# Performance work log

Hardware: AMD Instinct MI355X
Metric: run time of the kernel (lower is better)

## Reference

```python
import jax, jax.numpy as jnp
import numpy as np

N = 65536          # nodes
D = 64             # nclasses / head dim
H = 1              # num_heads (forward math requires H == 1)
NITER = 4
NITER_ATTN = 4
KHOP = 2           # npow_attn(=1, hard-coded) + 1
R = 1024           # row-chunk size in residual loss
DEG = 8            # out-degree before symmetrization


def setup_inputs():
    rng = np.random.default_rng(0)
    cols0 = rng.integers(0, N, size=N * DEG).astype(np.int32)
    rows0 = np.repeat(np.arange(N, dtype=np.int32), DEG)
    loop = np.arange(N, dtype=np.int32)
    rows = np.concatenate([rows0, cols0, loop])           # symmetrized + self-loops (A + I)
    cols = np.concatenate([cols0, rows0, loop])
    deg = np.bincount(rows, minlength=N).astype(np.float32)
    vals = (1.0 / np.sqrt(deg[rows] * deg[cols])).astype(np.float32)  # D^-1/2 (A+I) D^-1/2
    key = jax.random.key(0)
    ks = jax.random.split(key, 8)
    sc = 1.0 / np.sqrt(D)
    return {
        "local_preds": jax.random.normal(ks[0], (N, D), jnp.float32),
        "idx": jnp.arange(N, dtype=jnp.int32),
        "adj_rows": jnp.asarray(rows),
        "adj_cols": jnp.asarray(cols),
        "adj_vals": jnp.asarray(vals),
        "Wq_w": jax.random.normal(ks[1], (H * D, D), jnp.float32) * sc,
        "Wq_b": jax.random.normal(ks[2], (H * D,), jnp.float32) * sc,
        "Wk_w": jax.random.normal(ks[3], (H * D, D), jnp.float32) * sc,
        "Wk_b": jax.random.normal(ks[4], (H * D,), jnp.float32) * sc,
        "lin1_w": jax.random.normal(ks[5], (1, NITER), jnp.float32) * sc,
        "lin2_w": jax.random.normal(ks[6], (1, NITER_ATTN), jnp.float32) * sc,
    }


def _spmm(rows, cols, vals, x):
    # sparse (A+I)_norm @ x via gather + segment-sum
    return jax.ops.segment_sum(vals[:, None] * x[cols], rows, num_segments=N)


def _fro(x):
    return jnp.sqrt(jnp.sum(x * x))


def _on_attn(qn, kn, vs, n_norm):
    # On_attention_conv with pre-normalized qn/kn, K_hop = KHOP
    new_vs = vs
    for _ in range(KHOP):
        kv = jnp.einsum('lhm,lhd->hmd', kn, new_vs)
        new_vs = jnp.einsum('nhm,hmd->nhd', qn, kv)
    new_vs = new_vs + vs.sum(axis=0)[None]           # + vs_sum broadcast over rows
    normz = jnp.einsum('nhm,hm->nh', qn, kn.sum(axis=0))[..., None] + n_norm
    return new_vs / normz


def _forward(local_preds, adj_rows, adj_cols, adj_vals, Wq_w, Wq_b, Wk_w, Wk_b, lin1_w, lin2_w):
    preds = local_preds
    query = (preds @ Wq_w.T + Wq_b).reshape(N, H, D)
    key_t = (preds @ Wk_w.T + Wk_b).reshape(N, H, D)
    qn = query / _fro(query)   # global-Frobenius normalization (as in torch.norm(qs, p=2))
    kn = key_t / _fro(key_t)
    beta = lin2_w[0]           # [NITER_ATTN]
    alph = lin1_w[0]           # [NITER]

    # main Hop-Stack iteration (H == 1 collapses the head broadcasts)
    M_list = [preds]
    tmp = preds
    for _ in range(1, NITER):
        qk_list = [tmp]
        qk_tmp = tmp
        for _ in range(1, NITER_ATTN):
            qk_tmp = _on_attn(qn, kn, qk_tmp[:, None, :], N).mean(axis=1)
            qk_list.append(qk_tmp)
        mix = jnp.einsum('k,knd->nd', beta, jnp.stack(qk_list))
        tmp = _spmm(adj_rows, adj_cols, adj_vals, mix)
        M_list.append(tmp)
    preds_out = jnp.einsum('k,knd->nd', alph, jnp.stack(M_list))

    # residual loss (torch.no_grad, N > r branch), computed in closed form per row-chunk
    m2 = [query.mean(axis=1)]
    t = query.mean(axis=1)
    for _ in range(2, NITER_ATTN):
        o = _on_attn(qn, kn, t[:, None, :], N).mean(axis=1)
        t = _spmm(adj_rows, adj_cols, adj_vals, o)
        m2.append(t)
    gq = jnp.einsum('k,knd->nd', beta[1:], jnp.stack(m2))[:, None, :]  # GraphA_q [N,H,D]
    c = N // R
    s = jnp.sqrt(jnp.sum(gq.reshape(c, -1) ** 2, axis=1))       # per-chunk Frobenius norm of qs
    row_chunk = jnp.arange(N) // R
    qn2 = gq * (1.0 / s)[row_chunk][:, None, None]
    normz = jnp.einsum('nhm,hm->nh', qn2, kn.sum(axis=0)) + R   # [N,H]
    G = jnp.einsum('lhm,lhp->hmp', kn, kn)                      # key gram [H,D,D]
    # ||attn||_F^2 summed over all chunks, without materializing [R,H,N]
    t1 = jnp.sum(jnp.einsum('nhm,hmp,nhp->nh', qn2, G, qn2) / normz ** 2)
    c0 = beta[0] - 1.0
    dots = jnp.einsum('ehm,ehm->eh', qn2[adj_rows], kn[adj_cols])  # attn at sparse A entries
    t2 = 2.0 * c0 * jnp.sum(adj_vals[:, None] * dots / normz[adj_rows])
    t3 = c0 ** 2 * H * jnp.sum(adj_vals ** 2)
    loss = jnp.sqrt(t1 + t2 + t3)
    return preds_out, jax.lax.stop_gradient(loss)


def reference(local_preds, idx, adj_rows, adj_cols, adj_vals, Wq_w, Wq_b, Wk_w, Wk_b, lin1_w, lin2_w):
    del idx  # unused by the original forward body
    return _forward(local_preds, adj_rows, adj_cols, adj_vals, Wq_w, Wq_b, Wk_w, Wk_b, lin1_w, lin2_w)
```

## Files before the change

kernel.cpp:

```cpp
#include <hip/hip_runtime.h>

#define NN 65536
#define DD 64
#define ND (NN*DD)
#define E0 (NN*8)
#define B1 128
#define EPB (E0/B1)

enum {
  SM_ACC   = 0,
  SM_SCAL  = 4,
  SM_KSUM  = 24,
  SM_CHUNK = 96,
  SM_T2    = 160,
  SM_KQ    = 2208,
  SM_G     = SM_KQ + 4096,
  SM_C0    = SM_G + 4096,
  SM_H     = SM_C0 + 4240,
  SM_Z     = SM_H + 4096,
  SM_ZF    = SM_Z + 4160,
  SM_C     = SM_ZF + 4160,
  SM_CMIX  = SM_C + 4240,
  SM_CFIN  = SM_CMIX + 4240,
  SM_END   = SM_CFIN + 4240
};

#define GP 512
#define RP 512
#define QKP 1024
#define GRAM_STRIDE 12544

__device__ __forceinline__ void f4arr(float4 v, float* a){ a[0]=v.x; a[1]=v.y; a[2]=v.z; a[3]=v.w; }

__device__ __forceinline__ unsigned short f2bf(float f){
  union{float f;unsigned u;}v; v.f=f;
  unsigned r = v.u + 0x7fffu + ((v.u>>16)&1u);
  return (unsigned short)(r>>16);
}
__device__ __forceinline__ float bf2f(unsigned short h){
  union{unsigned u;float f;}v; v.u=((unsigned)h)<<16; return v.f;
}

__global__ __launch_bounds__(256,4) void k_qk(const float* __restrict__ preds,
    const float* __restrict__ Wq, const float* __restrict__ bq,
    const float* __restrict__ Wk, const float* __restrict__ bk,
    float* __restrict__ qout, float* __restrict__ kout, float* __restrict__ slab)
{
  __shared__ float sWq[64*68];
  __shared__ float sWk[64*68];
  __shared__ float sbq[64], sbk[64], sks[64];
  __shared__ float sred[8];
  int t = threadIdx.x;
  for (int i=t;i<4096;i+=256){ int d=i>>6, m=i&63; sWq[m*68+d]=Wq[i]; sWk[m*68+d]=Wk[i]; }
  if (t<64){ sbq[t]=bq[t]; sbk[t]=bk[t]; sks[t]=0.f; }
  __syncthreads();
  int td=t&15, g=t>>4, d0=td*4;
  int base = blockIdx.x*64;
  float aq[16], ak[16];
  #pragma unroll
  for (int i=0;i<4;i++)
    #pragma unroll
    for (int j=0;j<4;j++){ aq[i*4+j]=sbq[d0+j]; ak[i*4+j]=sbk[d0+j]; }
  const float4* pr0=(const float4*)(preds+(size_t)(base+g   )*DD);
  const float4* pr1=(const float4*)(preds+(size_t)(base+g+16)*DD);
  const float4* pr2=(const float4*)(preds+(size_t)(base+g+32)*DD);
  const float4* pr3=(const float4*)(preds+(size_t)(base+g+48)*DD);
  float4 pc0=pr0[0], pc1=pr1[0], pc2=pr2[0], pc3=pr3[0];
  for (int ms=0; ms<16; ms++){
    float4 pn0=pc0,pn1=pc1,pn2=pc2,pn3=pc3;
    if (ms<15){ pn0=pr0[ms+1]; pn1=pr1[ms+1]; pn2=pr2[ms+1]; pn3=pr3[ms+1]; }
    int m=ms*4;
    float wq[4][4], wk[4][4];
    #pragma unroll
    for (int k=0;k<4;k++){ f4arr(*(const float4*)&sWq[(m+k)*68+d0], wq[k]); f4arr(*(const float4*)&sWk[(m+k)*68+d0], wk[k]); }
    float p[4];
    f4arr(pc0,p);
    #pragma unroll
    for (int k=0;k<4;k++)
      #pragma unroll
      for (int j=0;j<4;j++){ aq[0*4+j]+=p[k]*wq[k][j]; ak[0*4+j]+=p[k]*wk[k][j]; }
    f4arr(pc1,p);
    #pragma unroll
    for (int k=0;k<4;k++)
      #pragma unroll
      for (int j=0;j<4;j++){ aq[1*4+j]+=p[k]*wq[k][j]; ak[1*4+j]+=p[k]*wk[k][j]; }
    f4arr(pc2,p);
    #pragma unroll
    for (int k=0;k<4;k++)
      #pragma unroll
      for (int j=0;j<4;j++){ aq[2*4+j]+=p[k]*wq[k][j]; ak[2*4+j]+=p[k]*wk[k][j]; }
    f4arr(pc3,p);
    #pragma unroll
    for (int k=0;k<4;k++)
      #pragma unroll
      for (int j=0;j<4;j++){ aq[3*4+j]+=p[k]*wq[k][j]; ak[3*4+j]+=p[k]*wk[k][j]; }
    pc0=pn0; pc1=pn1; pc2=pn2; pc3=pn3;
  }
  float ssq=0.f, ssk=0.f;
  #pragma unroll
  for (int i=0;i<4;i++){
    int r=base+g+16*i;
    float4 Q=make_float4(aq[i*4+0],aq[i*4+1],aq[i*4+2],aq[i*4+3]);
    float4 K=make_float4(ak[i*4+0],ak[i*4+1],ak[i*4+2],ak[i*4+3]);
    ((float4*)(qout+(size_t)r*DD))[td]=Q;
    ((float4*)(kout+(size_t)r*DD))[td]=K;
    ssq += Q.x*Q.x+Q.y*Q.y+Q.z*Q.z+Q.w*Q.w;
    ssk += K.x*K.x+K.y*K.y+K.z*K.z+K.w*K.w;
  }
  #pragma unroll
  for (int j=0;j<4;j++){
    float cs = ak[0*4+j]+ak[1*4+j]+ak[2*4+j]+ak[3*4+j];
    atomicAdd(&sks[d0+j], cs);
  }
  #pragma unroll
  for (int off=32;off;off>>=1){ ssq+=__shfl_down(ssq,off,64); ssk+=__shfl_down(ssk,off,64); }
  if ((t&63)==0){ sred[t>>6]=ssq; sred[4+(t>>6)]=ssk; }
  __syncthreads();
  float* my = slab + (size_t)blockIdx.x*66;
  if (t<64) my[t]=sks[t];
  if (t==0){ my[64]=sred[0]+sred[1]+sred[2]+sred[3]; my[65]=sred[4]+sred[5]+sred[6]+sred[7]; }
}

__global__ __launch_bounds__(256) void k_psumW(const float* __restrict__ slab, int stride, int n, int P,
                                               float* __restrict__ out)
{
  int col=blockIdx.x*4+(threadIdx.x>>6);
  int lane=threadIdx.x&63;
  if (col>=n) return;
  float a0=0.f,a1=0.f;
  int p=lane;
  for (; p+64<P; p+=128){ a0+=slab[(size_t)p*stride+col]; a1+=slab[(size_t)(p+64)*stride+col]; }
  for (; p<P; p+=64) a0+=slab[(size_t)p*stride+col];
  float a=a0+a1;
  #pragma unroll
  for (int off=32;off;off>>=1) a+=__shfl_down(a,off,64);
  if (lane==0) out[col]=a;
}

__global__ void k_scalars(float* __restrict__ ksum, float* __restrict__ sc, const float* __restrict__ lin2){
  __shared__ float s_ki;
  int t=threadIdx.x;
  if (t==0){
    float fq=sqrtf(ksum[64]), fk=sqrtf(ksum[65]);
    float qi=1.f/fq, ki=1.f/fk;
    sc[0]=qi; sc[1]=ki; sc[2]=qi*ki; sc[3]=lin2[1]*qi; sc[4]=1.f;
    sc[5]=ki;    sc[6]=1.f; sc[7]=qi;
    sc[8]=qi*ki; sc[9]=qi;  sc[10]=qi;
    s_ki=ki;
  }
  __syncthreads();
  if (t<64) ksum[t]*=s_ki;
}

__global__ __launch_bounds__(256) void k_gramc0p(const float* __restrict__ qn, const float* __restrict__ kn,
    const float* __restrict__ ksum, const float* __restrict__ sc,
    float* __restrict__ invn, float* __restrict__ slab)
{
  __shared__ float sk[16][64], sq[16][64], sw[16], sks[64];
  int t=threadIdx.x, tp=t&15, tm=t>>4;
  if (t<64) sks[t]=ksum[t];
  float qi_=sc[0];
  float akq[16], ag[16], ac0[16];
  #pragma unroll
  for (int i=0;i<16;i++){akq[i]=0.f;ag[i]=0.f;ac0[i]=0.f;}
  float rb[4]={0,0,0,0}, cb[4]={0,0,0,0}; float s22=0.f;
  for (int tile=blockIdx.x; tile<NN/16; tile+=gridDim.x){
    int base=tile*16;
    ((float4*)sk)[t]=((const float4*)(kn+(size_t)base*DD))[t];
    ((float4*)sq)[t]=((const float4*)(qn+(size_t)base*DD))[t];
    __syncthreads();
    {
      float p = sq[tm][tp]*sks[tp] + sq[tm][tp+16]*sks[tp+16]
              + sq[tm][tp+32]*sks[tp+32] + sq[tm][tp+48]*sks[tp+48];
      p += __shfl_xor(p,1,64); p += __shfl_xor(p,2,64);
      p += __shfl_xor(p,4,64); p += __shfl_xor(p,8,64);
      float w = 1.f/(p*qi_ + (float)NN);
      if (tp==0){ sw[tm]=w; invn[base+tm]=w; }
    }
    __syncthreads();
    #pragma unroll
    for (int r=0;r<16;r++){
      float w=sw[r];
      float km[4],qp[4],kp[4];
      f4arr(((const float4*)&sk[r][0])[tm], km);
      f4arr(((const float4*)&sq[r][0])[tp], qp);
      f4arr(((const float4*)&sk[r][0])[tp], kp);
      float wq[4]={w*qp[0],w*qp[1],w*qp[2],w*qp[3]};
      #pragma unroll
      for (int i=0;i<4;i++)
        #pragma unroll
        for (int j=0;j<4;j++){
          akq[i*4+j]+=km[i]*qp[j];
          ag [i*4+j]+=km[i]*kp[j];
          ac0[i*4+j]+=km[i]*wq[j];
        }
      if (tp==0){
        #pragma unroll
        for (int i=0;i<4;i++) rb[i]+=km[i]*w;
      }
      if (tm==0){
        #pragma unroll
        for (int j=0;j<4;j++) cb[j]+=wq[j];
      }
      if (t==0) s22+=w;
    }
    __syncthreads();
  }
  float* my = slab + (size_t)blockIdx.x*GRAM_STRIDE;
  #pragma unroll
  for (int i=0;i<4;i++)
    #pragma unroll
    for (int j=0;j<4;j++){
      my[       (tm*4+i)*DD+tp*4+j] = akq[i*4+j];
      my[4096 + (tm*4+i)*DD+tp*4+j] = ag [i*4+j];
      my[8192 + (tm*4+i)*65+tp*4+j] = ac0[i*4+j];
    }
  if (tp==0){
    #pragma unroll
    for (int i=0;i<4;i++) my[8192 + (tm*4+i)*65+64] = rb[i];
  }
  if (tm==0){
    #pragma unroll
    for (int j=0;j<4;j++) my[8192 + 64*65+tp*4+j] = cb[j];
  }
  if (t==0) my[8192 + 64*65+64] = s22;
}

__global__ void k_applyscale(float* __restrict__ KQ, float* __restrict__ G, float* __restrict__ C0,
                             const float* __restrict__ sc){
  int i=blockIdx.x*256+threadIdx.x;
  float qi=sc[0], ki=sc[1], qk=sc[2];
  if (i<4096){ KQ[i]*=qk; G[i]*=ki*ki; }
  if (i<4225){
    int a=i/65, b=i-65*a;
    float s = (a<64)? (b<64? qk : ki) : (b<64? qi : 1.f);
    C0[i]*=s;
  }
}

__global__ __launch_bounds__(256) void k_Hp(const float* __restrict__ q2, const float* __restrict__ wv,
                                            float* __restrict__ slab)
{
  __shared__ float sq[16][64], sw[16];
  int t=threadIdx.x, tp=t&15, tm=t>>4;
  float acc[16];
  #pragma unroll
  for (int i=0;i<16;i++) acc[i]=0.f;
  for (int tile=blockIdx.x; tile<NN/16; tile+=gridDim.x){
    int base=tile*16;
    ((float4*)sq)[t]=((const float4*)(q2+(size_t)base*DD))[t];
    if (t<16) sw[t]=wv[base+t];
    __syncthreads();
    #pragma unroll
    for (int r=0;r<16;r++){
      float w=sw[r]; w=w*w;
      float qm[4],qp[4];
      f4arr(((const float4*)&sq[r][0])[tm], qm);
      f4arr(((const float4*)&sq[r][0])[tp], qp);
      float wq[4]={w*qp[0],w*qp[1],w*qp[2],w*qp[3]};
      #pragma unroll
      for (int i=0;i<4;i++)
        #pragma unroll
        for (int j=0;j<4;j++) acc[i*4+j]+=qm[i]*wq[j];
    }
    __syncthreads();
  }
  float* my = slab + (size_t)blockIdx.x*4096;
  #pragma unroll
  for (int i=0;i<4;i++)
    #pragma unroll
    for (int j=0;j<4;j++) my[(tm*4+i)*DD+tp*4+j] = acc[i*4+j];
}

__global__ __launch_bounds__(256) void k_redp(const float* __restrict__ kn, const float* __restrict__ v,
                                              float* __restrict__ slab)
{
  __shared__ float sk[16][64], sv[16][64];
  int t=threadIdx.x, tp=t&15, tm=t>>4;
  float acc[16];
  #pragma unroll
  for (int i=0;i<16;i++) acc[i]=0.f;
  float cs[4]={0,0,0,0};
  for (int tile=blockIdx.x; tile<NN/16; tile+=gridDim.x){
    int base=tile*16;
    ((float4*)sk)[t]=((const float4*)(kn+(size_t)base*DD))[t];
    ((float4*)sv)[t]=((const float4*)(v+(size_t)base*DD))[t];
    __syncthreads();
    #pragma unroll
    for (int r=0;r<16;r++){
      float km[4],vd[4];
      f4arr(((const float4*)&sk[r][0])[tm], km);
      f4arr(((const float4*)&sv[r][0])[tp], vd);
      #pragma unroll
      for (int i=0;i<4;i++)
        #pragma unroll
        for (int j=0;j<4;j++) acc[i*4+j]+=km[i]*vd[j];
      if (tm==0){
        #pragma unroll
        for (int j=0;j<4;j++) cs[j]+=vd[j];
      }
    }
    __syncthreads();
  }
  float* my = slab + (size_t)blockIdx.x*4160;
  #pragma unroll
  for (int i=0;i<4;i++)
    #pragma unroll
    for (int j=0;j<4;j++) my[(tm*4+i)*DD+tp*4+j] = acc[i*4+j];
  if (tm==0){
    #pragma unroll
    for (int j=0;j<4;j++) my[64*DD+tp*4+j] = cs[j];
  }
}

__global__ void k_zfin(const float* __restrict__ Cfin, const float* __restrict__ z, float* __restrict__ zf,
                       const float* __restrict__ sc3){
  int a=blockIdx.x, d=threadIdx.x;
  float it=sc3[0], ib=sc3[1], ot=sc3[2];
  float acc=0.f;
  for (int b=0;b<64;b++) acc += Cfin[a*65+b]*z[b*DD+d];
  acc = acc*it + Cfin[a*65+64]*ib*z[64*DD+d];
  zf[a*DD+d] = (a<64? ot:1.f)*acc;
}
__global__ void k_zB(const float* __restrict__ KQ, const float* __restrict__ z, float* __restrict__ zf,
                     const float* __restrict__ sc3){
  int a=blockIdx.x, d=threadIdx.x;
  float it=sc3[0], ib=sc3[1], ot=sc3[2];
  float acc;
  if (a<64){ acc=0.f; for (int m=0;m<64;m++) acc += KQ[a*DD+m]*z[m*DD+d]; acc*=it*ot; }
  else acc = ib*z[64*DD+d];
  zf[a*DD+d]=acc;
}

__global__ __launch_bounds__(256) void k_expand(const float* __restrict__ qn,
    const float* __restrict__ Zf, const float* __restrict__ invn, const float* __restrict__ sdeg,
    const float* __restrict__ self, const float* __restrict__ coefp, int cidx,
    unsigned short* __restrict__ outv)
{
  __shared__ float sQ[64*68];
  __shared__ float sZ[65*64];
  int t=threadIdx.x;
  int base=blockIdx.x*64;
  for (int i=t;i<1040;i+=256) ((float4*)sZ)[i]=((const float4*)Zf)[i];
  for (int i=t;i<1024;i+=256){
    int r=i>>4, c4=i&15;
    float4 v=((const float4*)(qn+(size_t)(base+r)*DD))[c4];
    float* dst=&sQ[r*68+c4*4]; dst[0]=v.x;dst[1]=v.y;dst[2]=v.z;dst[3]=v.w;
  }
  __syncthreads();
  int td=t&15, g=t>>4, d0=td*4;
  float acc[16];
  {
    float ones[4]; f4arr(*(const float4*)&sZ[64*DD+d0], ones);
    #pragma unroll
    for (int i=0;i<4;i++)
      #pragma unroll
      for (int j=0;j<4;j++) acc[i*4+j]=ones[j];
  }
  for (int m=0;m<64;m+=4){
    float zr[4][4];
    #pragma unroll
    for (int k=0;k<4;k++) f4arr(*(const float4*)&sZ[(m+k)*DD+d0], zr[k]);
    #pragma unroll
    for (int i=0;i<4;i++){
      float p[4]; f4arr(*(const float4*)&sQ[(g+16*i)*68+m], p);
      #pragma unroll
      for (int k=0;k<4;k++)
        #pragma unroll
        for (int j=0;j<4;j++) acc[i*4+j]+=p[k]*zr[k][j];
    }
  }
  bool hasself=(cidx>=0);
  float cc = hasself ? coefp[cidx] : 0.f;
  #pragma unroll
  for (int i=0;i<4;i++){
    int r=base+g+16*i;
    float w=invn[r];
    float sd=sdeg[r];
    float4 o=make_float4(acc[i*4+0]*w,acc[i*4+1]*w,acc[i*4+2]*w,acc[i*4+3]*w);
    if (hasself){
      float4 s4=((const float4*)(self+(size_t)r*DD))[td];
      o.x+=cc*s4.x; o.y+=cc*s4.y; o.z+=cc*s4.z; o.w+=cc*s4.w;
    }
    o.x*=sd; o.y*=sd; o.z*=sd; o.w*=sd;
    ushort4 o4; o4.x=f2bf(o.x); o4.y=f2bf(o.y); o4.z=f2bf(o.z); o4.w=f2bf(o.w);
    ((ushort4*)(outv+(size_t)r*DD))[td]=o4;
  }
}

__global__ void k_makeC(const float* __restrict__ C0, const float* __restrict__ KQ, float* __restrict__ C){
  int a=blockIdx.x, d=threadIdx.x;
  float acc=0.f;
  for (int m=0;m<64;m++) acc += C0[a*65+m]*KQ[m*DD+d];
  C[a*65+d]=acc;
  if (d==0) C[a*65+64]=C0[a*65+64];
}
__global__ void k_makeCmix(const float* __restrict__ C, const float* __restrict__ lin2, float* __restrict__ Cmix){
  int a=blockIdx.x, c=threadIdx.x;
  if (c>=65) return;
  float b1=lin2[1], b2=lin2[2], b3=lin2[3];
  float acc=0.f;
  for (int b=0;b<65;b++) acc += C[a*65+b]*C[b*65+c];
  float r = b2*C[a*65+c] + b3*acc;
  if (a==c) r += b1;
  Cmix[a*65+c]=r;
}
__global__ void k_makeCfin(const float* __restrict__ KQ, const float* __restrict__ Cmix, float* __restrict__ Cfin){
  int a=blockIdx.x, c=threadIdx.x;
  if (c>=65) return;
  float acc;
  if (a<64){ acc=0.f; for (int m=0;m<64;m++) acc += KQ[a*DD+m]*Cmix[m*65+c]; }
  else acc = Cmix[64*65+c];
  Cfin[a*65+c]=acc;
}

__global__ __launch_bounds__(256) void k_hist2(const int* __restrict__ acols, unsigned int* __restrict__ slab){
  __shared__ unsigned int lc[16384];
  int t=threadIdx.x;
  for (int i=t;i<16384;i+=256) lc[i]=0u;
  __syncthreads();
  int e0=blockIdx.x*EPB;
  for (int i=t;i<EPB;i+=256){
    int c=acols[e0+i];
    atomicAdd(&lc[c>>2], 1u<<((c&3)*8));
  }
  __syncthreads();
  unsigned int* my=slab+(size_t)blockIdx.x*16384;
  for (int i=t;i<16384;i+=256) my[i]=lc[i];
}

__global__ __launch_bounds__(256) void k_pscan(unsigned int* __restrict__ slab, int* __restrict__ cnt,
                                               float* __restrict__ sdeg, float* __restrict__ accs){
  int w=blockIdx.x*256+threadIdx.x;
  unsigned int r0=0,r1=0,r2=0,r3=0;
  for (int b=0;b<B1;b++){
    unsigned int v=slab[(size_t)b*16384+w];
    slab[(size_t)b*16384+w] = r0|(r1<<8)|(r2<<16)|(r3<<24);
    r0+=v&255u; r1+=(v>>8)&255u; r2+=(v>>16)&255u; r3+=(v>>24)&255u;
  }
  ((int4*)cnt)[w]=make_int4((int)r0,(int)r1,(int)r2,(int)r3);
  float d0=(float)r0+9.f, d1=(float)r1+9.f, d2=(float)r2+9.f, d3=(float)r3+9.f;
  float s0=1.f/sqrtf(d0), s1=1.f/sqrtf(d1), s2=1.f/sqrtf(d2), s3=1.f/sqrtf(d3);
  ((float4*)sdeg)[w]=make_float4(s0,s1,s2,s3);
  float t3 = 1.f/(d0*d0)+1.f/(d1*d1)+1.f/(d2*d2)+1.f/(d3*d3);
  #pragma unroll
  for (int off=32;off;off>>=1) t3+=__shfl_down(t3,off,64);
  if ((threadIdx.x&63)==0) atomicAdd(&accs[1], t3);
}

__global__ __launch_bounds__(1024) void k_scan(const int* __restrict__ cnt, int* __restrict__ row_start){
  __shared__ int wtot[16];
  int t=threadIdx.x, lane=t&63, wid=t>>6;
  int base=t*64;
  int s=0;
  for (int i=0;i<64;i++) s+=cnt[base+i];
  int tot=s;
  for (int off=1;off<64;off<<=1){ int v=__shfl_up(s,off,64); if(lane>=off) s+=v; }
  if (lane==63) wtot[wid]=s;
  __syncthreads();
  if (t<16){
    int v=wtot[t];
    for (int off=1;off<16;off<<=1){ int u=__shfl_up(v,off,64); if(t>=off) v+=u; }
    wtot[t]=v;
  }
  __syncthreads();
  int excl = s - tot + (wid? wtot[wid-1]:0);
  int run=excl;
  for (int i=0;i<64;i++){ row_start[base+i]=run; run+=cnt[base+i]; }
  if (t==1023) row_start[NN]=run;
}

__global__ __launch_bounds__(256) void k_scatter2(const int* __restrict__ acols,
    const unsigned int* __restrict__ slab, const int* __restrict__ row_start,
    const float* __restrict__ sdeg, unsigned short* __restrict__ ccols16, float* __restrict__ accs){
  __shared__ unsigned int lc[16384];
  int t=threadIdx.x;
  for (int i=t;i<16384;i+=256) lc[i]=0u;
  __syncthreads();
  int e0=blockIdx.x*EPB;
  const unsigned int* my=slab+(size_t)blockIdx.x*16384;
  float t3=0.f;
  for (int i=t;i<EPB;i+=256){
    int e=e0+i;
    int c=acols[e];
    unsigned int sh=(unsigned int)(c&3)*8u;
    unsigned int old=atomicAdd(&lc[c>>2], 1u<<sh);
    unsigned int lp=(old>>sh)&255u;
    unsigned int pref=(my[c>>2]>>sh)&255u;
    int slot=row_start[c]+(int)pref+(int)lp;
    ccols16[slot]=(unsigned short)(e>>3);
    float sp=sdeg[e>>3]*sdeg[c];
    t3 += 2.f*sp*sp;
  }
  #pragma unroll
  for (int off=32;off;off>>=1) t3+=__shfl_down(t3,off,64);
  __shared__ float sred[4];
  if ((t&63)==0) sred[t>>6]=t3;
  __syncthreads();
  if (t==0) atomicAdd(&accs[1], sred[0]+sred[1]+sred[2]+sred[3]);
}

__global__ __launch_bounds__(256) void k_spmm2(const int* __restrict__ row_start,
    const unsigned short* __restrict__ ccols16, const int* __restrict__ acols,
    const float* __restrict__ sdeg,
    const unsigned short* __restrict__ xs, float* __restrict__ outv, int wout,
    float* __restrict__ accbuf, const float* __restrict__ coefp, int cidx,
    const float* __restrict__ initsrc, int initc, const float* __restrict__ iscale)
{
  int lane=threadIdx.x&63;
  int row=blockIdx.x*4+(threadIdx.x>>6);
  int s=row_start[row], e=row_start[row+1];
  int din=e-s;
  int dc=din>56?56:din;
  int L=8+dc;
  int myc=0;
  if (lane<8) myc=acols[row*8+lane];
  else if (lane<L) myc=(int)ccols16[s+lane-8];
  float a0=0,a1=0,a2=0,a3=0,a4=0,a5=0,a6=0,a7=0;
  int i=0;
  for (; i+8<=L; i+=8){
    int c0=__shfl(myc,i  ,64), c1=__shfl(myc,i+1,64), c2=__shfl(myc,i+2,64), c3=__shfl(myc,i+3,64);
    int c4=__shfl(myc,i+4,64), c5=__shfl(myc,i+5,64), c6=__shfl(myc,i+6,64), c7=__shfl(myc,i+7,64);
    float v0=bf2f(xs[(size_t)c0*DD+lane]), v1=bf2f(xs[(size_t)c1*DD+lane]);
    float v2=bf2f(xs[(size_t)c2*DD+lane]), v3=bf2f(xs[(size_t)c3*DD+lane]);
    float v4=bf2f(xs[(size_t)c4*DD+lane]), v5=bf2f(xs[(size_t)c5*DD+lane]);
    float v6=bf2f(xs[(size_t)c6*DD+lane]), v7=bf2f(xs[(size_t)c7*DD+lane]);
    a0+=v0; a1+=v1; a2+=v2; a3+=v3; a4+=v4; a5+=v5; a6+=v6; a7+=v7;
  }
  for (; i+4<=L; i+=4){
    int c0=__shfl(myc,i,64), c1=__shfl(myc,i+1,64), c2=__shfl(myc,i+2,64), c3=__shfl(myc,i+3,64);
    a0+=bf2f(xs[(size_t)c0*DD+lane]); a1+=bf2f(xs[(size_t)c1*DD+lane]);
    a2+=bf2f(xs[(size_t)c2*DD+lane]); a3+=bf2f(xs[(size_t)c3*DD+lane]);
  }
  for (; i<L; ++i){
    int c=__shfl(myc,i,64);
    a0 += bf2f(xs[(size_t)c*DD+lane]);
  }
  for (int j=56;j<din;j++){ int c=(int)ccols16[s+j]; a0+=bf2f(xs[(size_t)c*DD+lane]); }
  float acc=((a0+a1)+(a2+a3))+((a4+a5)+(a6+a7));
  acc += bf2f(xs[(size_t)row*DD+lane]);
  acc *= sdeg[row];
  size_t off=(size_t)row*DD+lane;
  if (wout) outv[off]=acc;
  if (cidx>=0){
    float cc=coefp[cidx];
    float base;
    if (initc>=0){
      float isc = iscale ? *iscale : coefp[initc];
      base = isc*initsrc[off];
    } else base = accbuf[off];
    accbuf[off]=base+cc*acc;
  }
}

__global__ __launch_bounds__(256) void k_scalerows(const float4* __restrict__ kn, const float* __restrict__ sdeg,
                                                   const float* __restrict__ sc, unsigned short* __restrict__ kns){
  float ki=sc[1];
  int i=blockIdx.x*256+threadIdx.x;
  int stride=gridDim.x*256;
  for (; i<ND/4; i+=stride){
    float sd=sdeg[i>>4]*ki;
    float4 v=kn[i];
    ushort4 o; o.x=f2bf(sd*v.x); o.y=f2bf(sd*v.y); o.z=f2bf(sd*v.z); o.w=f2bf(sd*v.w);
    ((ushort4*)kns)[i]=o;
  }
}

__global__ __launch_bounds__(256) void k_t2v(const int* __restrict__ row_start,
    const unsigned short* __restrict__ ccols16, const int* __restrict__ acols,
    const float* __restrict__ sdeg, const unsigned short* __restrict__ kns,
    const float* __restrict__ q2, const float* __restrict__ w, float* __restrict__ t2out)
{
  int lane=threadIdx.x&63;
  int wid=blockIdx.x*4+(threadIdx.x>>6);
  int nw=gridDim.x*4;
  float t=0.f;
  for (int row=wid; row<NN; row+=nw){
    int s=row_start[row], e=row_start[row+1];
    int din=e-s;
    int dc=din>56?56:din;
    int L=8+dc;
    int myc=0;
    if (lane<8) myc=acols[row*8+lane];
    else if (lane<L) myc=(int)ccols16[s+lane-8];
    float a0=0,a1=0,a2=0,a3=0,a4=0,a5=0,a6=0,a7=0;
    int i=0;
    for (; i+8<=L; i+=8){
      int c0=__shfl(myc,i  ,64), c1=__shfl(myc,i+1,64), c2=__shfl(myc,i+2,64), c3=__shfl(myc,i+3,64);
      int c4=__shfl(myc,i+4,64), c5=__shfl(myc,i+5,64), c6=__shfl(myc,i+6,64), c7=__shfl(myc,i+7,64);
      a0+=bf2f(kns[(size_t)c0*DD+lane]); a1+=bf2f(kns[(size_t)c1*DD+lane]);
      a2+=bf2f(kns[(size_t)c2*DD+lane]); a3+=bf2f(kns[(size_t)c3*DD+lane]);
      a4+=bf2f(kns[(size_t)c4*DD+lane]); a5+=bf2f(kns[(size_t)c5*DD+lane]);
      a6+=bf2f(kns[(size_t)c6*DD+lane]); a7+=bf2f(kns[(size_t)c7*DD+lane]);
    }
    for (; i+4<=L; i+=4){
      int c0=__shfl(myc,i,64), c1=__shfl(myc,i+1,64), c2=__shfl(myc,i+2,64), c3=__shfl(myc,i+3,64);
      a0+=bf2f(kns[(size_t)c0*DD+lane]); a1+=bf2f(kns[(size_t)c1*DD+lane]);
      a2+=bf2f(kns[(size_t)c2*DD+lane]); a3+=bf2f(kns[(size_t)c3*DD+lane]);
    }
    for (; i<L; ++i){
      int c=__shfl(myc,i,64);
      a0 += bf2f(kns[(size_t)c*DD+lane]);
    }
    for (int j=56;j<din;j++){ int c=(int)ccols16[s+j]; a0+=bf2f(kns[(size_t)c*DD+lane]); }
    float acc=((a0+a1)+(a2+a3))+((a4+a5)+(a6+a7));
    acc += bf2f(kns[(size_t)row*DD+lane]);
    t += w[row]*q2[(size_t)row*DD+lane]*sdeg[row]*acc;
  }
  #pragma unroll
  for (int off=32;off;off>>=1) t+=__shfl_down(t,off,64);
  __shared__ float sred[4];
  if ((threadIdx.x&63)==0) sred[threadIdx.x>>6]=t;
  __syncthreads();
  if (threadIdx.x==0) t2out[blockIdx.x]=sred[0]+sred[1]+sred[2]+sred[3];
}

__global__ __launch_bounds__(256) void k_chunk(const float* __restrict__ gq, float* __restrict__ chunk_inv){
  int c=blockIdx.x;
  const float4* p=(const float4*)(gq + (size_t)c*65536);
  float ss=0.f;
  for (int i=threadIdx.x;i<16384;i+=256){ float4 v=p[i]; ss += v.x*v.x+v.y*v.y+v.z*v.z+v.w*v.w; }
  __shared__ float red[4];
  #pragma unroll
  for (int off=32;off;off>>=1) ss+=__shfl_down(ss,off,64);
  if ((threadIdx.x&63)==0) red[threadIdx.x>>6]=ss;
  __syncthreads();
  if (threadIdx.x==0){ float s=red[0]+red[1]+red[2]+red[3]; chunk_inv[c]=1.f/sqrtf(s); }
}

__global__ __launch_bounds__(256) void k_nrm2(float* __restrict__ gq, const float* __restrict__ chunk_inv,
                                              const float* __restrict__ ks, float* __restrict__ nrm2inv){
  __shared__ float sks[64];
  if (threadIdx.x<64) sks[threadIdx.x]=ks[threadIdx.x];
  __syncthreads();
  int lane=threadIdx.x&63;
  int wid=blockIdx.x*4+(threadIdx.x>>6);
  int nw=gridDim.x*4;
  for (int row=wid;row<NN;row+=nw){
    float q=gq[(size_t)row*DD+lane]*chunk_inv[row>>10];
    gq[(size_t)row*DD+lane]=q;
    float p=q*sks[lane];
    #pragma unroll
    for (int off=32;off;off>>=1) p+=__shfl_down(p,off,64);
    if (lane==0) nrm2inv[row]=1.f/(p+1024.f);
  }
}

__global__ void k_final(const float* __restrict__ G, const float* __restrict__ H,
                        const float* __restrict__ t2s, const float* __restrict__ accs,
                        const float* __restrict__ lin2, float* __restrict__ outv){
  __shared__ float red[256];
  __shared__ float gh;
  int t=threadIdx.x;
  float s=0.f;
  for (int i=t;i<4096;i+=256) s+=G[i]*H[i];
  red[t]=s;
  __syncthreads();
  for (int k=128;k;k>>=1){ if (t<k) red[t]+=red[t+k]; __syncthreads(); }
  if (t==0) gh=red[0];
  __syncthreads();
  float s2=0.f;
  for (int i=t;i<2048;i+=256) s2+=t2s[i];
  red[t]=s2;
  __syncthreads();
  for (int k=128;k;k>>=1){ if (t<k) red[t]+=red[t+k]; __syncthreads(); }
  if (t==0){
    float c0=lin2[0]-1.f;
    outv[0]=sqrtf(gh + 2.f*c0*red[0] + c0*c0*accs[1]);
  }
}

extern "C" void kernel_launch(void* const* d_in, const int* in_sizes, int n_in,
                              void* d_out, int out_size, void* d_ws, size_t ws_size,
                              hipStream_t stream)
{
  (void)n_in; (void)out_size; (void)ws_size; (void)in_sizes;
  const float* preds = (const float*)d_in[0];
  const int*   acols = (const int*)d_in[3];
  const float* Wq    = (const float*)d_in[5];
  const float* bq    = (const float*)d_in[6];
  const float* Wk    = (const float*)d_in[7];
  const float* bk    = (const float*)d_in[8];
  const float* lin1  = (const float*)d_in[9];
  const float* lin2  = (const float*)d_in[10];
  float* outp = (float*)d_out;

  float* W    = (float*)d_ws;
  float* q    = W;
  float* k    = W + (size_t)ND;
  float* tmpM = W + 2*(size_t)ND;
  unsigned short* mixh = (unsigned short*)(W + 3*(size_t)ND);
  float* bufv = W + 3*(size_t)ND + ND/2;
  float* invn = bufv + (size_t)ND;
  float* sdeg = invn + NN;
  float* sm   = sdeg + NN;
  int* cnt       = (int*)(sm + SM_END);
  int* row_start = cnt + NN;
  unsigned short* ccols16 = (unsigned short*)(row_start + NN + 1);
  float* slab = (float*)(ccols16 + E0);

  unsigned int* hist_slab = (unsigned int*)tmpM;
  unsigned short* knsh = mixh;

  float* sc=sm+SM_SCAL;
  float* KQ=sm+SM_KQ; float* G=sm+SM_G; float* H=sm+SM_H;
  float* z=sm+SM_Z; float* zf=sm+SM_ZF;
  float* C0=sm+SM_C0; float* C=sm+SM_C; float* Cmix=sm+SM_CMIX; float* Cfin=sm+SM_CFIN;

  hipMemsetAsync(sm, 0, 24*sizeof(float), stream);

  k_qk<<<QKP,256,0,stream>>>(preds,Wq,bq,Wk,bk,q,k,slab);
  k_psumW<<<(66+3)/4,256,0,stream>>>(slab, 66, 66, QKP, sm+SM_KSUM);
  k_scalars<<<1,64,0,stream>>>(sm+SM_KSUM, sc, lin2);
  k_gramc0p<<<GP,256,0,stream>>>(q,k,sm+SM_KSUM,sc,invn,slab);
  k_psumW<<<(12417+3)/4,256,0,stream>>>(slab, GRAM_STRIDE, 12417, GP, KQ);
  k_applyscale<<<17,256,0,stream>>>(KQ,G,C0,sc);
  k_makeC<<<65,64,0,stream>>>(C0,KQ,C);
  k_makeCmix<<<65,128,0,stream>>>(C,lin2,Cmix);
  k_makeCfin<<<65,128,0,stream>>>(KQ,Cmix,Cfin);

  k_hist2<<<B1,256,0,stream>>>(acols, hist_slab);
  k_pscan<<<64,256,0,stream>>>(hist_slab, cnt, sdeg, sm+SM_ACC);
  k_scan<<<1,1024,0,stream>>>(cnt, row_start);
  k_scatter2<<<B1,256,0,stream>>>(acols, hist_slab, row_start, sdeg, ccols16, sm+SM_ACC);

  for (int i=1;i<4;i++){
    const float* v = (i==1) ? preds : tmpM;
    k_redp<<<RP,256,0,stream>>>(k,v,slab);
    k_psumW<<<(4160+3)/4,256,0,stream>>>(slab, 4160, 4160, RP, z);
    k_zfin<<<65,64,0,stream>>>(Cfin,z,zf, sc+5);
    k_expand<<<1024,256,0,stream>>>(q,zf,invn,sdeg,v,lin2,0,mixh);
    if (i==1)
      k_spmm2<<<16384,256,0,stream>>>(row_start,ccols16,acols,sdeg,mixh,tmpM,1,outp,lin1,1,preds,0,nullptr);
    else
      k_spmm2<<<16384,256,0,stream>>>(row_start,ccols16,acols,sdeg,mixh,tmpM,1,outp,lin1,i,nullptr,-1,nullptr);
  }

  k_redp<<<RP,256,0,stream>>>(k,q,slab);
  k_psumW<<<(4160+3)/4,256,0,stream>>>(slab, 4160, 4160, RP, z);
  k_zB<<<65,64,0,stream>>>(KQ,z,zf, sc+8);
  k_expand<<<1024,256,0,stream>>>(q,zf,invn,sdeg,nullptr,nullptr,-1,mixh);
  k_spmm2<<<16384,256,0,stream>>>(row_start,ccols16,acols,sdeg,mixh,bufv,1,tmpM,lin2,2,q,1,sc+3);
  k_redp<<<RP,256,0,stream>>>(k,bufv,slab);
  k_psumW<<<(4160+3)/4,256,0,stream>>>(slab, 4160, 4160, RP, z);
  k_zB<<<65,64,0,stream>>>(KQ,z,zf, sc+5);
  k_expand<<<1024,256,0,stream>>>(q,zf,invn,sdeg,nullptr,nullptr,-1,mixh);
  k_spmm2<<<16384,256,0,stream>>>(row_start,ccols16,acols,sdeg,mixh,nullptr,0,tmpM,lin2,3,nullptr,-1,nullptr);

  k_chunk<<<64,256,0,stream>>>(tmpM, sm+SM_CHUNK);
  k_nrm2<<<2048,256,0,stream>>>(tmpM, sm+SM_CHUNK, sm+SM_KSUM, invn);
  k_scalerows<<<1024,256,0,stream>>>((const float4*)k, sdeg, sc, knsh);
  k_Hp<<<RP,256,0,stream>>>(tmpM, invn, slab);
  k_psumW<<<(4096+3)/4,256,0,stream>>>(slab, 4096, 4096, RP, H);
  k_t2v<<<2048,256,0,stream>>>(row_start,ccols16,acols,sdeg,knsh,tmpM,invn,sm+SM_T2);
  k_final<<<1,256,0,stream>>>(G,H,sm+SM_T2,sm+SM_ACC,lin2,outp+ND);
}
```

Measured before the change: 786.8 us.

## Process two rows per wave in SpMM gathers and stream q from registers in expand

The SpMM and t2 gather kernels now assign two rows per 64-lane wave, each half-wave reading bf16 pairs (ushort2) per lane. Padding lanes point to a zeroed dummy row at index NN instead of being skipped, so both halves can iterate to the larger of their two lengths. The grid shrinks accordingly, and the workspace is shifted to make room for the dummy row. k_expand drops its shared-memory q tile and loads q rows straight from global memory with register prefetch, adding an occupancy hint. The aim is fewer idle lanes on short rows, wider loads and less LDS traffic, at the cost of wasted gathers on the zero row when the two rows' degrees differ.

```diff
diff --git a/kernel.cpp b/kernel.cpp
--- a/kernel.cpp
+++ b/kernel.cpp
@@ -332,23 +332,17 @@
   zf[a*DD+d]=acc;
 }
 
-__global__ __launch_bounds__(256) void k_expand(const float* __restrict__ qn,
+__global__ __launch_bounds__(256,4) void k_expand(const float* __restrict__ qn,
     const float* __restrict__ Zf, const float* __restrict__ invn, const float* __restrict__ sdeg,
     const float* __restrict__ self, const float* __restrict__ coefp, int cidx,
     unsigned short* __restrict__ outv)
 {
-  __shared__ float sQ[64*68];
   __shared__ float sZ[65*64];
   int t=threadIdx.x;
+  for (int i=t;i<1040;i+=256) ((float4*)sZ)[i]=((const float4*)Zf)[i];
+  __syncthreads();
+  int td=t&15, g=t>>4, d0=td*4;
   int base=blockIdx.x*64;
-  for (int i=t;i<1040;i+=256) ((float4*)sZ)[i]=((const float4*)Zf)[i];
-  for (int i=t;i<1024;i+=256){
-    int r=i>>4, c4=i&15;
-    float4 v=((const float4*)(qn+(size_t)(base+r)*DD))[c4];
-    float* dst=&sQ[r*68+c4*4]; dst[0]=v.x;dst[1]=v.y;dst[2]=v.z;dst[3]=v.w;
-  }
-  __syncthreads();
-  int td=t&15, g=t>>4, d0=td*4;
   float acc[16];
   {
     float ones[4]; f4arr(*(const float4*)&sZ[64*DD+d0], ones);
@@ -357,18 +351,40 @@
       #pragma unroll
       for (int j=0;j<4;j++) acc[i*4+j]=ones[j];
   }
-  for (int m=0;m<64;m+=4){
+  const float4* pr0=(const float4*)(qn+(size_t)(base+g   )*DD);
+  const float4* pr1=(const float4*)(qn+(size_t)(base+g+16)*DD);
+  const float4* pr2=(const float4*)(qn+(size_t)(base+g+32)*DD);
+  const float4* pr3=(const float4*)(qn+(size_t)(base+g+48)*DD);
+  float4 pc0=pr0[0], pc1=pr1[0], pc2=pr2[0], pc3=pr3[0];
+  for (int ms=0; ms<16; ms++){
+    float4 pn0=pc0,pn1=pc1,pn2=pc2,pn3=pc3;
+    if (ms<15){ pn0=pr0[ms+1]; pn1=pr1[ms+1]; pn2=pr2[ms+1]; pn3=pr3[ms+1]; }
+    int m=ms*4;
     float zr[4][4];
     #pragma unroll
     for (int k=0;k<4;k++) f4arr(*(const float4*)&sZ[(m+k)*DD+d0], zr[k]);
-    #pragma unroll
-    for (int i=0;i<4;i++){
-      float p[4]; f4arr(*(const float4*)&sQ[(g+16*i)*68+m], p);
-      #pragma unroll
-      for (int k=0;k<4;k++)
-        #pragma unroll
-        for (int j=0;j<4;j++) acc[i*4+j]+=p[k]*zr[k][j];
-    }
+    float p[4];
+    f4arr(pc0,p);
+    #pragma unroll
+    for (int k=0;k<4;k++)
+      #pragma unroll
+      for (int j=0;j<4;j++) acc[0*4+j]+=p[k]*zr[k][j];
+    f4arr(pc1,p);
+    #pragma unroll
+    for (int k=0;k<4;k++)
+      #pragma unroll
+      for (int j=0;j<4;j++) acc[1*4+j]+=p[k]*zr[k][j];
+    f4arr(pc2,p);
+    #pragma unroll
+    for (int k=0;k<4;k++)
+      #pragma unroll
+      for (int j=0;j<4;j++) acc[2*4+j]+=p[k]*zr[k][j];
+    f4arr(pc3,p);
+    #pragma unroll
+    for (int k=0;k<4;k++)
+      #pragma unroll
+      for (int j=0;j<4;j++) acc[3*4+j]+=p[k]*zr[k][j];
+    pc0=pn0; pc1=pn1; pc2=pn2; pc3=pn3;
   }
   bool hasself=(cidx>=0);
   float cc = hasself ? coefp[cidx] : 0.f;
@@ -508,48 +524,64 @@
     const float* __restrict__ initsrc, int initc, const float* __restrict__ iscale)
 {
   int lane=threadIdx.x&63;
-  int row=blockIdx.x*4+(threadIdx.x>>6);
+  int h=lane>>5, l32=lane&31;
+  int wv=(blockIdx.x*256+threadIdx.x)>>6;
+  int row=wv*2+h;
   int s=row_start[row], e=row_start[row+1];
   int din=e-s;
-  int dc=din>56?56:din;
-  int L=8+dc;
-  int myc=0;
-  if (lane<8) myc=acols[row*8+lane];
-  else if (lane<L) myc=(int)ccols16[s+lane-8];
-  float a0=0,a1=0,a2=0,a3=0,a4=0,a5=0,a6=0,a7=0;
+  int dpre=din>24?24:din;
+  int L=8+dpre;
+  int myc=NN;
+  if (l32<8) myc=acols[row*8+l32];
+  else if (l32<L) myc=(int)ccols16[s+l32-8];
+  int Lo=__shfl(L, lane^32, 64);
+  int Lmax=L>Lo?L:Lo;
+  int bs=h*32;
+  float ax0=0,ay0=0,ax1=0,ay1=0,ax2=0,ay2=0,ax3=0,ay3=0;
   int i=0;
-  for (; i+8<=L; i+=8){
-    int c0=__shfl(myc,i  ,64), c1=__shfl(myc,i+1,64), c2=__shfl(myc,i+2,64), c3=__shfl(myc,i+3,64);
-    int c4=__shfl(myc,i+4,64), c5=__shfl(myc,i+5,64), c6=__shfl(myc,i+6,64), c7=__shfl(myc,i+7,64);
-    float v0=bf2f(xs[(size_t)c0*DD+lane]), v1=bf2f(xs[(size_t)c1*DD+lane]);
-    float v2=bf2f(xs[(size_t)c2*DD+lane]), v3=bf2f(xs[(size_t)c3*DD+lane]);
-    float v4=bf2f(xs[(size_t)c4*DD+lane]), v5=bf2f(xs[(size_t)c5*DD+lane]);
-    float v6=bf2f(xs[(size_t)c6*DD+lane]), v7=bf2f(xs[(size_t)c7*DD+lane]);
-    a0+=v0; a1+=v1; a2+=v2; a3+=v3; a4+=v4; a5+=v5; a6+=v6; a7+=v7;
-  }
-  for (; i+4<=L; i+=4){
-    int c0=__shfl(myc,i,64), c1=__shfl(myc,i+1,64), c2=__shfl(myc,i+2,64), c3=__shfl(myc,i+3,64);
-    a0+=bf2f(xs[(size_t)c0*DD+lane]); a1+=bf2f(xs[(size_t)c1*DD+lane]);
-    a2+=bf2f(xs[(size_t)c2*DD+lane]); a3+=bf2f(xs[(size_t)c3*DD+lane]);
-  }
-  for (; i<L; ++i){
-    int c=__shfl(myc,i,64);
-    a0 += bf2f(xs[(size_t)c*DD+lane]);
-  }
-  for (int j=56;j<din;j++){ int c=(int)ccols16[s+j]; a0+=bf2f(xs[(size_t)c*DD+lane]); }
-  float acc=((a0+a1)+(a2+a3))+((a4+a5)+(a6+a7));
-  acc += bf2f(xs[(size_t)row*DD+lane]);
-  acc *= sdeg[row];
-  size_t off=(size_t)row*DD+lane;
-  if (wout) outv[off]=acc;
+  for (; i+4<=Lmax; i+=4){
+    int c0=__shfl(myc,bs+i  ,64), c1=__shfl(myc,bs+i+1,64);
+    int c2=__shfl(myc,bs+i+2,64), c3=__shfl(myc,bs+i+3,64);
+    ushort2 u0=*(const ushort2*)(xs+(size_t)c0*DD+2*l32);
+    ushort2 u1=*(const ushort2*)(xs+(size_t)c1*DD+2*l32);
+    ushort2 u2=*(const ushort2*)(xs+(size_t)c2*DD+2*l32);
+    ushort2 u3=*(const ushort2*)(xs+(size_t)c3*DD+2*l32);
+    ax0+=bf2f(u0.x); ay0+=bf2f(u0.y);
+    ax1+=bf2f(u1.x); ay1+=bf2f(u1.y);
+    ax2+=bf2f(u2.x); ay2+=bf2f(u2.y);
+    ax3+=bf2f(u3.x); ay3+=bf2f(u3.y);
+  }
+  for (; i<Lmax; ++i){
+    int c=__shfl(myc,bs+i,64);
+    ushort2 u=*(const ushort2*)(xs+(size_t)c*DD+2*l32);
+    ax0+=bf2f(u.x); ay0+=bf2f(u.y);
+  }
+  for (int j=24;j<din;j++){
+    int c=(int)ccols16[s+j];
+    ushort2 u=*(const ushort2*)(xs+(size_t)c*DD+2*l32);
+    ax0+=bf2f(u.x); ay0+=bf2f(u.y);
+  }
+  {
+    ushort2 u=*(const ushort2*)(xs+(size_t)row*DD+2*l32);
+    ax0+=bf2f(u.x); ay0+=bf2f(u.y);
+  }
+  float sd=sdeg[row];
+  float ox=((ax0+ax1)+(ax2+ax3))*sd;
+  float oy=((ay0+ay1)+(ay2+ay3))*sd;
+  size_t off=(size_t)row*DD+2*l32;
+  if (wout) *(float2*)(outv+off)=make_float2(ox,oy);
   if (cidx>=0){
     float cc=coefp[cidx];
-    float base;
+    float bx,by;
     if (initc>=0){
       float isc = iscale ? *iscale : coefp[initc];
-      base = isc*initsrc[off];
-    } else base = accbuf[off];
-    accbuf[off]=base+cc*acc;
+      float2 iv=*(const float2*)(initsrc+off);
+      bx=isc*iv.x; by=isc*iv.y;
+    } else {
+      float2 av=*(const float2*)(accbuf+off);
+      bx=av.x; by=av.y;
+    }
+    *(float2*)(accbuf+off)=make_float2(bx+cc*ox, by+cc*oy);
   }
 }
 
@@ -572,40 +604,55 @@
     const float* __restrict__ q2, const float* __restrict__ w, float* __restrict__ t2out)
 {
   int lane=threadIdx.x&63;
-  int wid=blockIdx.x*4+(threadIdx.x>>6);
-  int nw=gridDim.x*4;
+  int h=lane>>5, l32=lane&31;
+  int wv=(blockIdx.x*256+threadIdx.x)>>6;
+  int nwv=gridDim.x*4;
   float t=0.f;
-  for (int row=wid; row<NN; row+=nw){
+  for (int pr=wv; pr<NN/2; pr+=nwv){
+    int row=pr*2+h;
     int s=row_start[row], e=row_start[row+1];
     int din=e-s;
-    int dc=din>56?56:din;
-    int L=8+dc;
-    int myc=0;
-    if (lane<8) myc=acols[row*8+lane];
-    else if (lane<L) myc=(int)ccols16[s+lane-8];
-    float a0=0,a1=0,a2=0,a3=0,a4=0,a5=0,a6=0,a7=0;
+    int dpre=din>24?24:din;
+    int L=8+dpre;
+    int myc=NN;
+    if (l32<8) myc=acols[row*8+l32];
+    else if (l32<L) myc=(int)ccols16[s+l32-8];
+    int Lo=__shfl(L, lane^32, 64);
+    int Lmax=L>Lo?L:Lo;
+    int bs=h*32;
+    float ax0=0,ay0=0,ax1=0,ay1=0,ax2=0,ay2=0,ax3=0,ay3=0;
     int i=0;
-    for (; i+8<=L; i+=8){
-      int c0=__shfl(myc,i  ,64), c1=__shfl(myc,i+1,64), c2=__shfl(myc,i+2,64), c3=__shfl(myc,i+3,64);
-      int c4=__shfl(myc,i+4,64), c5=__shfl(myc,i+5,64), c6=__shfl(myc,i+6,64), c7=__shfl(myc,i+7,64);
-      a0+=bf2f(kns[(size_t)c0*DD+lane]); a1+=bf2f(kns[(size_t)c1*DD+lane]);
-      a2+=bf2f(kns[(size_t)c2*DD+lane]); a3+=bf2f(kns[(size_t)c3*DD+lane]);
-      a4+=bf2f(kns[(size_t)c4*DD+lane]); a5+=bf2f(kns[(size_t)c5*DD+lane]);
-      a6+=bf2f(kns[(size_t)c6*DD+lane]); a7+=bf2f(kns[(size_t)c7*DD+lane]);
-    }
-    for (; i+4<=L; i+=4){
-      int c0=__shfl(myc,i,64), c1=__shfl(myc,i+1,64), c2=__shfl(myc,i+2,64), c3=__shfl(myc,i+3,64);
-      a0+=bf2f(kns[(size_t)c0*DD+lane]); a1+=bf2f(kns[(size_t)c1*DD+lane]);
-      a2+=bf2f(kns[(size_t)c2*DD+lane]); a3+=bf2f(kns[(size_t)c3*DD+lane]);
-    }
-    for (; i<L; ++i){
-      int c=__shfl(myc,i,64);
-      a0 += bf2f(kns[(size_t)c*DD+lane]);
-    }
-    for (int j=56;j<din;j++){ int c=(int)ccols16[s+j]; a0+=bf2f(kns[(size_t)c*DD+lane]); }
-    float acc=((a0+a1)+(a2+a3))+((a4+a5)+(a6+a7));
-    acc += bf2f(kns[(size_t)row*DD+lane]);
-    t += w[row]*q2[(size_t)row*DD+lane]*sdeg[row]*acc;
+    for (; i+4<=Lmax; i+=4){
+      int c0=__shfl(myc,bs+i  ,64), c1=__shfl(myc,bs+i+1,64);
+      int c2=__shfl(myc,bs+i+2,64), c3=__shfl(myc,bs+i+3,64);
+      ushort2 u0=*(const ushort2*)(kns+(size_t)c0*DD+2*l32);
+      ushort2 u1=*(const ushort2*)(kns+(size_t)c1*DD+2*l32);
+      ushort2 u2=*(const ushort2*)(kns+(size_t)c2*DD+2*l32);
+      ushort2 u3=*(const ushort2*)(kns+(size_t)c3*DD+2*l32);
+      ax0+=bf2f(u0.x); ay0+=bf2f(u0.y);
+      ax1+=bf2f(u1.x); ay1+=bf2f(u1.y);
+      ax2+=bf2f(u2.x); ay2+=bf2f(u2.y);
+      ax3+=bf2f(u3.x); ay3+=bf2f(u3.y);
+    }
+    for (; i<Lmax; ++i){
+      int c=__shfl(myc,bs+i,64);
+      ushort2 u=*(const ushort2*)(kns+(size_t)c*DD+2*l32);
+      ax0+=bf2f(u.x); ay0+=bf2f(u.y);
+    }
+    for (int j=24;j<din;j++){
+      int c=(int)ccols16[s+j];
+      ushort2 u=*(const ushort2*)(kns+(size_t)c*DD+2*l32);
+      ax0+=bf2f(u.x); ay0+=bf2f(u.y);
+    }
+    {
+      ushort2 u=*(const ushort2*)(kns+(size_t)row*DD+2*l32);
+      ax0+=bf2f(u.x); ay0+=bf2f(u.y);
+    }
+    float sd=sdeg[row];
+    float ox=((ax0+ax1)+(ax2+ax3))*sd;
+    float oy=((ay0+ay1)+(ay2+ay3))*sd;
+    float2 qv=*(const float2*)(q2+(size_t)row*DD+2*l32);
+    t += w[row]*(qv.x*ox + qv.y*oy);
   }
   #pragma unroll
   for (int off=32;off;off>>=1) t+=__shfl_down(t,off,64);
@@ -690,7 +737,7 @@
   float* k    = W + (size_t)ND;
   float* tmpM = W + 2*(size_t)ND;
   unsigned short* mixh = (unsigned short*)(W + 3*(size_t)ND);
-  float* bufv = W + 3*(size_t)ND + ND/2;
+  float* bufv = W + 3*(size_t)ND + ND/2 + 32;
   float* invn = bufv + (size_t)ND;
   float* sdeg = invn + NN;
   float* sm   = sdeg + NN;
@@ -708,6 +755,7 @@
   float* C0=sm+SM_C0; float* C=sm+SM_C; float* Cmix=sm+SM_CMIX; float* Cfin=sm+SM_CFIN;
 
   hipMemsetAsync(sm, 0, 24*sizeof(float), stream);
+  hipMemsetAsync(mixh + (size_t)ND, 0, DD*2, stream);
 
   k_qk<<<QKP,256,0,stream>>>(preds,Wq,bq,Wk,bk,q,k,slab);
   k_psumW<<<(66+3)/4,256,0,stream>>>(slab, 66, 66, QKP, sm+SM_KSUM);
@@ -731,21 +779,21 @@
     k_zfin<<<65,64,0,stream>>>(Cfin,z,zf, sc+5);
     k_expand<<<1024,256,0,stream>>>(q,zf,invn,sdeg,v,lin2,0,mixh);
     if (i==1)
-      k_spmm2<<<16384,256,0,stream>>>(row_start,ccols16,acols,sdeg,mixh,tmpM,1,outp,lin1,1,preds,0,nullptr);
+      k_spmm2<<<NN/8,256,0,stream>>>(row_start,ccols16,acols,sdeg,mixh,tmpM,1,outp,lin1,1,preds,0,nullptr);
     else
-      k_spmm2<<<16384,256,0,stream>>>(row_start,ccols16,acols,sdeg,mixh,tmpM,1,outp,lin1,i,nullptr,-1,nullptr);
+      k_spmm2<<<NN/8,256,0,stream>>>(row_start,ccols16,acols,sdeg,mixh,tmpM,1,outp,lin1,i,nullptr,-1,nullptr);
   }
 
   k_redp<<<RP,256,0,stream>>>(k,q,slab);
   k_psumW<<<(4160+3)/4,256,0,stream>>>(slab, 4160, 4160, RP, z);
   k_zB<<<65,64,0,stream>>>(KQ,z,zf, sc+8);
   k_expand<<<1024,256,0,stream>>>(q,zf,invn,sdeg,nullptr,nullptr,-1,mixh);
-  k_spmm2<<<16384,256,0,stream>>>(row_start,ccols16,acols,sdeg,mixh,bufv,1,tmpM,lin2,2,q,1,sc+3);
+  k_spmm2<<<NN/8,256,0,stream>>>(row_start,ccols16,acols,sdeg,mixh,bufv,1,tmpM,lin2,2,q,1,sc+3);
   k_redp<<<RP,256,0,stream>>>(k,bufv,slab);
   k_psumW<<<(4160+3)/4,256,0,stream>>>(slab, 4160, 4160, RP, z);
   k_zB<<<65,64,0,stream>>>(KQ,z,zf, sc+5);
   k_expand<<<1024,256,0,stream>>>(q,zf,invn,sdeg,nullptr,nullptr,-1,mixh);
-  k_spmm2<<<16384,256,0,stream>>>(row_start,ccols16,acols,sdeg,mixh,nullptr,0,tmpM,lin2,3,nullptr,-1,nullptr);
+  k_spmm2<<<NN/8,256,0,stream>>>(row_start,ccols16,acols,sdeg,mixh,nullptr,0,tmpM,lin2,3,nullptr,-1,nullptr);
 
   k_chunk<<<64,256,0,stream>>>(tmpM, sm+SM_CHUNK);
   k_nrm2<<<2048,256,0,stream>>>(tmpM, sm+SM_CHUNK, sm+SM_KSUM, invn);
```

Result: slower. 2.150 ms (+173.3%).
